# Performance work log

Hardware: AMD Instinct MI355X
Metric: run time of the kernel (lower is better)

Reference implementation:

```python
import jax, jax.numpy as jnp
import numpy as np

V, T, E, H, L = 32000, 1024, 1024, 16, 6
D = E // H
FF = 4 * E
B = 2


def _ln(x, s, b, eps=1e-5):
    m = x.mean(-1, keepdims=True)
    v = x.var(-1, keepdims=True)
    return (x - m) * jax.lax.rsqrt(v + eps) * s + b


def setup_inputs() -> dict:
    key = jax.random.key(0)
    ks = jax.random.split(key, 16)
    std = 0.02
    inp = {
        "idx": jax.random.randint(ks[0], (B, T), 0, V),
        "tok_w": jax.random.normal(ks[1], (V, E)) * std,
        "pos_emb": jax.random.normal(ks[2], (1, T, E)) * std,
        # stacked per-layer params [L, ...]
        "ln1_s": jnp.ones((L, E)), "ln1_b": jnp.zeros((L, E)),
        "wq": jax.random.normal(ks[3], (L, E, E)) * std,
        "wk": jax.random.normal(ks[4], (L, E, E)) * std,
        "wv": jax.random.normal(ks[5], (L, E, E)) * std,
        "wo": jax.random.normal(ks[6], (L, E, E)) * std,
        "bo": jnp.zeros((L, E)),
        "ln2_s": jnp.ones((L, E)), "ln2_b": jnp.zeros((L, E)),
        "w1": jax.random.normal(ks[7], (L, E, FF)) * std,
        "b1": jnp.zeros((L, FF)),
        "w2": jax.random.normal(ks[8], (L, FF, E)) * std,
        "b2": jnp.zeros((L, E)),
        "lnf_s": jnp.ones((E,)), "lnf_b": jnp.zeros((E,)),
        "head_w": jax.random.normal(ks[9], (E, V)) * std,
        "head_b": jnp.zeros((V,)),
    }
    return inp


def _gpt(idx, tok_w, pos_emb, ln1_s, ln1_b, wq, wk, wv, wo, bo,
         ln2_s, ln2_b, w1, b1, w2, b2, lnf_s, lnf_b, head_w, head_b):
    x = tok_w[idx] + pos_emb[0, :T]                      # [B,T,E]
    mask = jnp.tril(jnp.ones((T, T), dtype=bool))        # causal mask
    scale = 1.0 / np.sqrt(D)

    def step(x, p):
        l1s, l1b, q_w, k_w, v_w, o_w, o_b, l2s, l2b, f1, fb1, f2, fb2 = p
        h = _ln(x, l1s, l1b)
        q = (h @ q_w).reshape(B, T, H, D)
        k = (h @ k_w).reshape(B, T, H, D)
        v = (h @ v_w).reshape(B, T, H, D)
        att = jnp.einsum('bthd,bshd->bhts', q, k) * scale  # [B,H,T,T]
        att = jnp.where(mask, att, -jnp.inf)
        att = jax.nn.softmax(att, axis=-1)
        o = jnp.einsum('bhts,bshd->bthd', att, v).reshape(B, T, E)
        x = x + o @ o_w + o_b
        h2 = _ln(x, l2s, l2b)
        x = x + jax.nn.relu(h2 @ f1 + fb1) @ f2 + fb2
        return x, None

    params = (ln1_s, ln1_b, wq, wk, wv, wo, bo, ln2_s, ln2_b, w1, b1, w2, b2)
    x, _ = jax.lax.scan(step, x, params)
    x = _ln(x, lnf_s, lnf_b)
    return x @ head_w + head_b                           # logits [B,T,V]


def reference(idx, tok_w, pos_emb, ln1_s, ln1_b, wq, wk, wv, wo, bo,
              ln2_s, ln2_b, w1, b1, w2, b2, lnf_s, lnf_b, head_w, head_b):
    return _gpt(idx, tok_w, pos_emb, ln1_s, ln1_b, wq, wk, wv, wo, bo,
                ln2_s, ln2_b, w1, b1, w2, b2, lnf_s, lnf_b, head_w, head_b)
```

## Files before the change

### kernel.cpp

```cpp
#include <hip/hip_runtime.h>


#define T_SEQ 1024
#define E_DIM 1024
#define H_NUM 16
#define D_HEAD 64
#define L_NUM 6
#define FF_DIM 4096
#define B_NUM 2
#define M_ROWS 2048

using bf16x8 = __attribute__((ext_vector_type(8))) __bf16;
using f32x4  = __attribute__((ext_vector_type(4))) float;

__device__ __forceinline__ unsigned short f2bf(float f) {
  unsigned int u = __float_as_uint(f);
  u += 0x7fffu + ((u >> 16) & 1u);
  return (unsigned short)(u >> 16);
}

__device__ __forceinline__ void gload_lds16(const void* g, void* l) {
  __builtin_amdgcn_global_load_lds(
      (const __attribute__((address_space(1))) unsigned int*)g,
      (__attribute__((address_space(3))) unsigned int*)l, 16, 0, 0);
}

__global__ __launch_bounds__(256) void embed_k(const int* __restrict__ idx,
                                               const float* __restrict__ tok_w,
                                               const float* __restrict__ pos,
                                               float* __restrict__ x) {
  const int i = blockIdx.x;
  const int t = i & (T_SEQ - 1);
  const int tok = idx[i];
  const float4 a = ((const float4*)(tok_w + (size_t)tok * E_DIM))[threadIdx.x];
  const float4 p = ((const float4*)(pos + (size_t)t * E_DIM))[threadIdx.x];
  float4 o;
  o.x = a.x + p.x; o.y = a.y + p.y; o.z = a.z + p.z; o.w = a.w + p.w;
  ((float4*)(x + (size_t)i * E_DIM))[threadIdx.x] = o;
}

__device__ __forceinline__ void ln_body(const float* __restrict__ x,
                                        const float* __restrict__ s,
                                        const float* __restrict__ b,
                                        unsigned short* __restrict__ out,
                                        int blk) {
  const int wave = threadIdx.x >> 6, lane = threadIdx.x & 63;
  const int row = blk * 4 + wave;
  const float4* xr = (const float4*)(x + (size_t)row * E_DIM);
  float4 v[4];
  float sum = 0.f, sq = 0.f;
  #pragma unroll
  for (int i = 0; i < 4; ++i) {
    v[i] = xr[lane + 64 * i];
    sum += v[i].x + v[i].y + v[i].z + v[i].w;
    sq  += v[i].x * v[i].x + v[i].y * v[i].y + v[i].z * v[i].z + v[i].w * v[i].w;
  }
  #pragma unroll
  for (int off = 1; off < 64; off <<= 1) {
    sum += __shfl_xor(sum, off);
    sq  += __shfl_xor(sq, off);
  }
  const float mean = sum * (1.0f / E_DIM);
  const float var  = sq * (1.0f / E_DIM) - mean * mean;
  const float inv  = 1.0f / sqrtf(var + 1e-5f);
  unsigned short* orow = out + (size_t)row * E_DIM;
  #pragma unroll
  for (int i = 0; i < 4; ++i) {
    const float4 sv = ((const float4*)s)[lane + 64 * i];
    const float4 bv = ((const float4*)b)[lane + 64 * i];
    ushort4 o;
    o.x = f2bf((v[i].x - mean) * inv * sv.x + bv.x);
    o.y = f2bf((v[i].y - mean) * inv * sv.y + bv.y);
    o.z = f2bf((v[i].z - mean) * inv * sv.z + bv.z);
    o.w = f2bf((v[i].w - mean) * inv * sv.w + bv.w);
    *(ushort4*)(orow + 4 * (lane + 64 * i)) = o;
  }
}

__global__ __launch_bounds__(256) void ln_k(const float* __restrict__ x,
                                            const float* __restrict__ s,
                                            const float* __restrict__ b,
                                            unsigned short* __restrict__ out) {
  ln_body(x, s, b, out, blockIdx.x);
}

__device__ __forceinline__ void trans_body(const float* __restrict__ W,
                                           unsigned short* __restrict__ WT,
                                           int K, int N, int b,
                                           float (*tile)[33]) {
  const int nbn = N >> 5;
  const int n0 = (b % nbn) << 5, k0 = (b / nbn) << 5;
  const int tx = threadIdx.x & 31, ty = threadIdx.x >> 5;
  #pragma unroll
  for (int i = ty; i < 32; i += 8)
    tile[i][tx] = W[(size_t)(k0 + i) * N + n0 + tx];
  __syncthreads();
  #pragma unroll
  for (int i = ty; i < 32; i += 8)
    WT[(size_t)(n0 + i) * K + k0 + tx] = f2bf(tile[tx][i]);
}

__global__ __launch_bounds__(256) void ln_trans_k(
    const float* __restrict__ x, const float* __restrict__ s,
    const float* __restrict__ b, unsigned short* __restrict__ outh,
    const float* __restrict__ wq, const float* __restrict__ wk,
    const float* __restrict__ wv, const float* __restrict__ wo,
    const float* __restrict__ w1, const float* __restrict__ w2,
    unsigned short* __restrict__ wt_qkv, unsigned short* __restrict__ wt_o,
    unsigned short* __restrict__ wt_f1, unsigned short* __restrict__ wt_f2) {
  __shared__ float tile[32][33];
  const int bid = blockIdx.x;
  if (bid < 512) { ln_body(x, s, b, outh, bid); return; }
  const int tb = bid - 512;
  if (tb < 3072) {
    const int w = tb >> 10;
    const float* W = (w == 0) ? wq : (w == 1) ? wk : wv;
    trans_body(W, wt_qkv + (size_t)w * 1024 * 1024, 1024, 1024, tb & 1023, tile);
  } else if (tb < 4096) {
    trans_body(wo, wt_o, 1024, 1024, tb - 3072, tile);
  } else if (tb < 8192) {
    trans_body(w1, wt_f1, 1024, 4096, tb - 4096, tile);
  } else {
    trans_body(w2, wt_f2, 4096, 1024, tb - 8192, tile);
  }
}

__global__ __launch_bounds__(256) void lnf_trans_k(
    const float* __restrict__ x, const float* __restrict__ s,
    const float* __restrict__ b, unsigned short* __restrict__ outh,
    const float* __restrict__ head_w, unsigned short* __restrict__ wth) {
  __shared__ float tile[32][33];
  const int bid = blockIdx.x;
  if (bid < 512) { ln_body(x, s, b, outh, bid); return; }
  trans_body(head_w, wth, 1024, 32000, bid - 512, tile);
}

template<int BM, bool RELU, bool BIAS, bool RES, bool OBF16>
__global__ __launch_bounds__(256) void gemm_k(const unsigned short* __restrict__ A,
                                              const unsigned short* __restrict__ WT,
                                              const float* __restrict__ bias,
                                              const float* __restrict__ res,
                                              void* __restrict__ Cout,
                                              int ldc, int K) {
  constexpr int BN = 128;
  constexpr int BK = 64;
  constexpr int MF = BM / 32;
  constexpr int AJ = (BM * BK * 2 / 1024) / 4;
  constexpr int BJ = (BN * BK * 2 / 1024) / 4;
  constexpr int NL = AJ + BJ;
  __shared__ __align__(16) unsigned short As[2][BM][BK];
  __shared__ __align__(16) unsigned short Bs[2][BN][BK];
  const int tid = threadIdx.x;
  const int row0 = blockIdx.x * BM, col0 = blockIdx.y * BN;
  const int wave = tid >> 6, lane = tid & 63;
  const int wm = (wave >> 1) * (BM / 2), wn = (wave & 1) * 64;
  const int lr = lane & 15, lg = lane >> 4;
  const int ric = lane >> 3, sslot = lane & 7;

  auto stage = [&](int buf, int k0) {
    #pragma unroll
    for (int j = 0; j < AJ; ++j) {
      const int c = wave + 4 * j;
      const int row = c * 8 + ric;
      const int sp = sslot ^ (row & 7);
      gload_lds16(A + (size_t)(row0 + row) * K + k0 + sp * 8,
                  (char*)&As[buf][0][0] + c * 1024);
    }
    #pragma unroll
    for (int j = 0; j < BJ; ++j) {
      const int c = wave + 4 * j;
      const int row = c * 8 + ric;
      const int sp = sslot ^ (row & 7);
      gload_lds16(WT + (size_t)(col0 + row) * K + k0 + sp * 8,
                  (char*)&Bs[buf][0][0] + c * 1024);
    }
  };

  f32x4 acc[MF][4] = {};
  const int nt = K / BK;
  stage(0, 0);
  asm volatile("s_waitcnt vmcnt(0)" ::: "memory");
  __builtin_amdgcn_s_barrier();
  for (int t = 0; t < nt; ++t) {
    const int cur = t & 1;
    if (t + 1 < nt) {
      stage(cur ^ 1, (t + 1) * BK);
      asm volatile("s_waitcnt vmcnt(%0)" :: "i"(NL) : "memory");
    } else {
      asm volatile("s_waitcnt vmcnt(0)" ::: "memory");
    }
    __builtin_amdgcn_s_barrier();
    #pragma unroll
    for (int ks = 0; ks < 2; ++ks) {
      bf16x8 af[MF], bfr[4];
      #pragma unroll
      for (int m = 0; m < MF; ++m) {
        const int r = wm + m * 16 + lr;
        const int s = (ks * 4 + lg) ^ (r & 7);
        af[m] = *(const bf16x8*)((const char*)&As[cur][0][0] + r * 128 + s * 16);
      }
      #pragma unroll
      for (int n = 0; n < 4; ++n) {
        const int r = wn + n * 16 + lr;
        const int s = (ks * 4 + lg) ^ (r & 7);
        bfr[n] = *(const bf16x8*)((const char*)&Bs[cur][0][0] + r * 128 + s * 16);
      }
      #pragma unroll
      for (int m = 0; m < MF; ++m)
        #pragma unroll
        for (int n = 0; n < 4; ++n)
          acc[m][n] = __builtin_amdgcn_mfma_f32_16x16x32_bf16(af[m], bfr[n], acc[m][n], 0, 0, 0);
    }
    __builtin_amdgcn_s_barrier();
  }
  float* Cf = (float*)Cout;
  unsigned short* Cb = (unsigned short*)Cout;
  #pragma unroll
  for (int m = 0; m < MF; ++m) {
    #pragma unroll
    for (int n = 0; n < 4; ++n) {
      const int col = col0 + wn + (n << 4) + lr;
      const float bv = BIAS ? bias[col] : 0.0f;
      #pragma unroll
      for (int r = 0; r < 4; ++r) {
        const int row = row0 + wm + (m << 4) + (lg << 2) + r;
        float val = acc[m][n][r] + bv;
        if (RELU) val = fmaxf(val, 0.0f);
        if (RES)  val += res[(size_t)row * ldc + col];
        if (OBF16) Cb[(size_t)row * ldc + col] = f2bf(val);
        else       Cf[(size_t)row * ldc + col] = val;
      }
    }
  }
}

#define LOAD_AF(HALF)                                                         \
  _Pragma("unroll")                                                           \
  for (int mf = 0; mf < 4; ++mf) {                                            \
    const int rr = wm * 64 + mf * 16 + lr;                                    \
    _Pragma("unroll")                                                         \
    for (int ks = 0; ks < 2; ++ks)                                            \
      af[mf][ks] = *(const bf16x8*)&As[buf][HALF][rr]                         \
          [(((ks << 2) + lgp) ^ (rr & 7)) << 3];                              \
  }
#define LOAD_BF(HALF, DST)                                                    \
  _Pragma("unroll")                                                           \
  for (int nf = 0; nf < 2; ++nf) {                                            \
    const int rr = wn * 32 + nf * 16 + lr;                                    \
    _Pragma("unroll")                                                         \
    for (int ks = 0; ks < 2; ++ks)                                            \
      DST[nf][ks] = *(const bf16x8*)&Bs[buf][HALF][rr]                        \
          [(((ks << 2) + lgp) ^ (rr & 7)) << 3];                              \
  }
#define MFMA_Q(MH, NH, BQ)                                                    \
  __builtin_amdgcn_s_setprio(1);                                              \
  _Pragma("unroll")                                                           \
  for (int mf = 0; mf < 4; ++mf)                                              \
    _Pragma("unroll")                                                         \
    for (int nf = 0; nf < 2; ++nf) {                                          \
      acc[MH][NH][mf][nf] = __builtin_amdgcn_mfma_f32_16x16x32_bf16(          \
          af[mf][0], BQ[nf][0], acc[MH][NH][mf][nf], 0, 0, 0);                \
      acc[MH][NH][mf][nf] = __builtin_amdgcn_mfma_f32_16x16x32_bf16(          \
          af[mf][1], BQ[nf][1], acc[MH][NH][mf][nf], 0, 0, 0);                \
    }                                                                         \
  __builtin_amdgcn_s_setprio(0);

__global__ __launch_bounds__(512) void gemm8_k(
    const unsigned short* __restrict__ A, const unsigned short* __restrict__ WT,
    const float* __restrict__ bias, float* __restrict__ C,
    int ldc, int K, int mgrid) {
  constexpr int BK = 64;
  __shared__ __align__(16) unsigned short As[2][2][128][64];
  __shared__ __align__(16) unsigned short Bs[2][2][128][64];
  const int tid = threadIdx.x;
  const int wave = tid >> 6, lane = tid & 63;
  const int wm = wave >> 2, wn = wave & 3;
  const int lr = lane & 15, lgp = lane >> 4;
  const int nwg = gridDim.x;
  const int q = nwg >> 3, r = nwg & 7;
  const int xcd = blockIdx.x & 7;
  const int lgid = (xcd < r ? xcd * (q + 1) : r * (q + 1) + (xcd - r) * q)
                   + (blockIdx.x >> 3);
  const int row0 = (lgid % mgrid) * 256, col0 = (lgid / mgrid) * 256;
  const int srow = lane >> 3, sslot = lane & 7;

  auto stA = [&](int buf, int half, int k0) {
    #pragma unroll
    for (int j = 0; j < 2; ++j) {
      const int row = j * 64 + wave * 8 + srow;
      const int sp = sslot ^ (row & 7);
      gload_lds16(A + (size_t)(row0 + half * 128 + row) * K + k0 + sp * 8,
                  (char*)&As[buf][half][0][0] + j * 8192 + wave * 1024);
    }
  };
  auto stB = [&](int buf, int half, int k0) {
    #pragma unroll
    for (int j = 0; j < 2; ++j) {
      const int row = j * 64 + wave * 8 + srow;
      const int sp = sslot ^ (row & 7);
      gload_lds16(WT + (size_t)(col0 + half * 128 + row) * K + k0 + sp * 8,
                  (char*)&Bs[buf][half][0][0] + j * 8192 + wave * 1024);
    }
  };

  f32x4 acc[2][2][4][2] = {};
  bf16x8 af[4][2], bfq0[2][2], bfq1[2][2];
  const int nt = K / BK;

  stA(0, 0, 0); stB(0, 1, 0); stB(0, 0, 0); stA(0, 1, 0);
  if (nt > 1) {
    stA(1, 0, BK); stB(1, 1, BK);
    asm volatile("s_waitcnt vmcnt(4)" ::: "memory");
  } else {
    asm volatile("s_waitcnt vmcnt(0)" ::: "memory");
  }
  __builtin_amdgcn_s_barrier();

  for (int t = 0; t < nt; ++t) {
    const int buf = t & 1, nbuf = buf ^ 1;
    const int k0 = t * BK;
    LOAD_AF(0)
    LOAD_BF(0, bfq0)
    if (t + 1 < nt) { stB(nbuf, 0, k0 + BK); stA(nbuf, 1, k0 + BK); }
    MFMA_Q(0, 0, bfq0)
    LOAD_BF(1, bfq1)
    MFMA_Q(0, 1, bfq1)
    __builtin_amdgcn_s_barrier();
    LOAD_AF(1)
    if (t + 2 < nt) stA(buf, 0, k0 + 2 * BK);
    MFMA_Q(1, 1, bfq1)
    if (t + 2 < nt) stB(buf, 1, k0 + 2 * BK);
    MFMA_Q(1, 0, bfq0)
    if (t + 1 < nt) {
      if (t + 2 < nt) asm volatile("s_waitcnt vmcnt(4)" ::: "memory");
      else            asm volatile("s_waitcnt vmcnt(0)" ::: "memory");
    }
    __builtin_amdgcn_s_barrier();
  }

  #pragma unroll
  for (int mh = 0; mh < 2; ++mh)
    #pragma unroll
    for (int nh = 0; nh < 2; ++nh)
      #pragma unroll
      for (int mf = 0; mf < 4; ++mf)
        #pragma unroll
        for (int nf = 0; nf < 2; ++nf) {
          const int col = col0 + nh * 128 + wn * 32 + nf * 16 + lr;
          const float bv = bias[col];
          #pragma unroll
          for (int rr = 0; rr < 4; ++rr) {
            const int row = row0 + mh * 128 + wm * 64 + mf * 16 + lgp * 4 + rr;
            C[(size_t)row * ldc + col] = acc[mh][nh][mf][nf][rr] + bv;
          }
        }
}

#define QBLK 128
#define KBLK 64
__global__ __launch_bounds__(512) void fattn_k(const unsigned short* __restrict__ qkv,
                                               unsigned short* __restrict__ ob) {
  const int qt = (T_SEQ / QBLK - 1) - blockIdx.x;
  const int h = blockIdx.y, b = blockIdx.z;
  const int tid = threadIdx.x;
  const int wave = tid >> 6, lane = tid & 63;
  const int lr = lane & 15, lg = lane >> 4;
  const int q0 = qt * QBLK;

  __shared__ __align__(16) unsigned short Qs[QBLK][72];
  __shared__ __align__(16) unsigned short Ks[2][KBLK][64];
  __shared__ __align__(16) unsigned short Vt[2][D_HEAD][72];
  __shared__ __align__(16) unsigned short Ps[QBLK][72];

  const size_t base = (size_t)b * T_SEQ * 3072 + (size_t)h * 64;
  const int srow = tid >> 3, scol = (tid & 7) << 3;
  const int krow = wave * 8 + (lane >> 3);
  const int ksp  = (lane & 7) ^ (krow & 7);

  uint4 vreg;
  auto stage_k = [&](int buf, int s0) {
    gload_lds16(qkv + base + 1024 + (size_t)(s0 + krow) * 3072 + ksp * 8,
                (char*)&Ks[buf][0][0] + wave * 1024);
  };
  auto load_v = [&](int s0) {
    vreg = *(const uint4*)(qkv + base + 2048 + (size_t)(s0 + srow) * 3072 + scol);
  };
  auto write_v = [&](int buf) {
    const unsigned short* ws = (const unsigned short*)&vreg;
    #pragma unroll
    for (int j = 0; j < 8; ++j) Vt[buf][scol + j][srow] = ws[j];
  };

  #pragma unroll
  for (int it = 0; it < 2; ++it) {
    const int row = srow + it * 64;
    *(uint4*)&Qs[row][scol] =
        *(const uint4*)(qkv + base + (size_t)(q0 + row) * 3072 + scol);
  }
  stage_k(0, 0);
  load_v(0);
  write_v(0);
  __syncthreads();
  bf16x8 qf[2];
  #pragma unroll
  for (int ks = 0; ks < 2; ++ks)
    qf[ks] = *(const bf16x8*)&Qs[wave * 16 + lr][ks * 32 + lg * 8];

  f32x4 acc_o[4] = {};
  float mrow[4], lrow[4];
  #pragma unroll
  for (int r = 0; r < 4; ++r) { mrow[r] = -3.0e38f; lrow[r] = 0.f; }

  const int ntile = 2 * (qt + 1);
  for (int kt = 0; kt < ntile; ++kt) {
    const int s0 = kt * KBLK;
    const int cur = kt & 1;
    f32x4 sacc[4] = {};
    __builtin_amdgcn_s_setprio(1);
    #pragma unroll
    for (int ks = 0; ks < 2; ++ks) {
      #pragma unroll
      for (int nf = 0; nf < 4; ++nf) {
        const int r = nf * 16 + lr;
        bf16x8 kf = *(const bf16x8*)((const char*)&Ks[cur][0][0] +
                                     r * 128 + (((ks << 2) + lg) ^ (r & 7)) * 16);
        sacc[nf] = __builtin_amdgcn_mfma_f32_16x16x32_bf16(qf[ks], kf, sacc[nf], 0, 0, 0);
      }
    }
    __builtin_amdgcn_s_setprio(0);
    if (kt + 1 < ntile) { stage_k(cur ^ 1, s0 + KBLK); load_v(s0 + KBLK); }
    float sv[4][4];
    #pragma unroll
    for (int nf = 0; nf < 4; ++nf)
      #pragma unroll
      for (int r = 0; r < 4; ++r) sv[nf][r] = sacc[nf][r] * 0.125f;
    if (s0 + KBLK - 1 > q0) {
      #pragma unroll
      for (int nf = 0; nf < 4; ++nf) {
        const int s = s0 + nf * 16 + lr;
        #pragma unroll
        for (int r = 0; r < 4; ++r) {
          const int qq = q0 + wave * 16 + lg * 4 + r;
          if (s > qq) sv[nf][r] = -3.0e38f;
        }
      }
    }
    float p[4][4];
    #pragma unroll
    for (int r = 0; r < 4; ++r) {
      float mx = fmaxf(fmaxf(sv[0][r], sv[1][r]), fmaxf(sv[2][r], sv[3][r]));
      #pragma unroll
      for (int off = 1; off < 16; off <<= 1) mx = fmaxf(mx, __shfl_xor(mx, off));
      const float mnew = fmaxf(mrow[r], mx);
      const float alpha = __expf(mrow[r] - mnew);
      mrow[r] = mnew;
      float sum = 0.f;
      #pragma unroll
      for (int nf = 0; nf < 4; ++nf) {
        p[nf][r] = __expf(sv[nf][r] - mnew);
        sum += p[nf][r];
      }
      #pragma unroll
      for (int off = 1; off < 16; off <<= 1) sum += __shfl_xor(sum, off);
      lrow[r] = lrow[r] * alpha + sum;
      #pragma unroll
      for (int df = 0; df < 4; ++df) acc_o[df][r] *= alpha;
    }
    #pragma unroll
    for (int nf = 0; nf < 4; ++nf)
      #pragma unroll
      for (int r = 0; r < 4; ++r)
        Ps[wave * 16 + lg * 4 + r][nf * 16 + lr] = f2bf(p[nf][r]);
    __builtin_amdgcn_s_setprio(1);
    #pragma unroll
    for (int ks = 0; ks < 2; ++ks) {
      bf16x8 pa = *(const bf16x8*)&Ps[wave * 16 + lr][ks * 32 + lg * 8];
      #pragma unroll
      for (int df = 0; df < 4; ++df) {
        bf16x8 vf = *(const bf16x8*)&Vt[cur][df * 16 + lr][ks * 32 + lg * 8];
        acc_o[df] = __builtin_amdgcn_mfma_f32_16x16x32_bf16(pa, vf, acc_o[df], 0, 0, 0);
      }
    }
    __builtin_amdgcn_s_setprio(0);
    if (kt + 1 < ntile) write_v(cur ^ 1);
    __syncthreads();
  }
  #pragma unroll
  for (int r = 0; r < 4; ++r) {
    const float inv = 1.0f / lrow[r];
    const int row = q0 + wave * 16 + lg * 4 + r;
    #pragma unroll
    for (int df = 0; df < 4; ++df)
      ob[((size_t)b * T_SEQ + row) * E_DIM + h * 64 + df * 16 + lr] =
          f2bf(acc_o[df][r] * inv);
  }
}

extern "C" void kernel_launch(void* const* d_in, const int* in_sizes, int n_in,
                              void* d_out, int out_size, void* d_ws, size_t ws_size,
                              hipStream_t stream) {
  (void)in_sizes; (void)n_in; (void)out_size; (void)ws_size;
  const int*   idx    = (const int*)d_in[0];
  const float* tok_w  = (const float*)d_in[1];
  const float* pos    = (const float*)d_in[2];
  const float* ln1_s  = (const float*)d_in[3];
  const float* ln1_b  = (const float*)d_in[4];
  const float* wq     = (const float*)d_in[5];
  const float* wk     = (const float*)d_in[6];
  const float* wv     = (const float*)d_in[7];
  const float* wo     = (const float*)d_in[8];
  const float* bo     = (const float*)d_in[9];
  const float* ln2_s  = (const float*)d_in[10];
  const float* ln2_b  = (const float*)d_in[11];
  const float* w1     = (const float*)d_in[12];
  const float* b1     = (const float*)d_in[13];
  const float* w2     = (const float*)d_in[14];
  const float* b2     = (const float*)d_in[15];
  const float* lnf_s  = (const float*)d_in[16];
  const float* lnf_b  = (const float*)d_in[17];
  const float* head_w = (const float*)d_in[18];
  const float* head_b = (const float*)d_in[19];
  float* out = (float*)d_out;

  char* p = (char*)d_ws;
  float* x            = (float*)p;          p += (size_t)M_ROWS * E_DIM * 4;
  unsigned short* qkvb= (unsigned short*)p; p += (size_t)M_ROWS * 3072 * 2;
  unsigned short* h   = (unsigned short*)p; p += (size_t)M_ROWS * E_DIM * 2;
  unsigned short* obuf= (unsigned short*)p; p += (size_t)M_ROWS * E_DIM * 2;
  unsigned short* ff  = (unsigned short*)p; p += (size_t)M_ROWS * FF_DIM * 2;
  unsigned short* wt  = (unsigned short*)p; p += (size_t)3072 * E_DIM * 2;
  unsigned short* wto = (unsigned short*)p; p += (size_t)E_DIM * E_DIM * 2;
  unsigned short* wtf1= (unsigned short*)p; p += (size_t)FF_DIM * E_DIM * 2;
  unsigned short* wtf2= (unsigned short*)p; p += (size_t)E_DIM * FF_DIM * 2;
  unsigned short* wth = (unsigned short*)p; p += (size_t)32000 * E_DIM * 2;

  embed_k<<<M_ROWS, 256, 0, stream>>>(idx, tok_w, pos, x);

  for (int l = 0; l < L_NUM; ++l) {
    const size_t lEE = (size_t)l * E_DIM * E_DIM;
    const size_t lEF = (size_t)l * E_DIM * FF_DIM;
    ln_trans_k<<<12800, 256, 0, stream>>>(
        x, ln1_s + l * E_DIM, ln1_b + l * E_DIM, h,
        wq + lEE, wk + lEE, wv + lEE, wo + lEE, w1 + lEF, w2 + lEF,
        wt, wto, wtf1, wtf2);
    gemm_k<64,false,false,false,true><<<dim3(32, 24), 256, 0, stream>>>(
        h, wt, nullptr, nullptr, qkvb, 3072, E_DIM);
    fattn_k<<<dim3(T_SEQ / QBLK, H_NUM, B_NUM), 512, 0, stream>>>(qkvb, obuf);
    gemm_k<32,false,true,true,false><<<dim3(64, 8), 256, 0, stream>>>(
        obuf, wto, bo + l * E_DIM, x, x, E_DIM, E_DIM);
    ln_k<<<M_ROWS / 4, 256, 0, stream>>>(x, ln2_s + l * E_DIM, ln2_b + l * E_DIM, h);
    gemm_k<64,true,true,false,true><<<dim3(32, 32), 256, 0, stream>>>(
        h, wtf1, b1 + l * FF_DIM, nullptr, ff, FF_DIM, E_DIM);
    gemm_k<32,false,true,true,false><<<dim3(64, 8), 256, 0, stream>>>(
        ff, wtf2, b2 + l * E_DIM, x, x, E_DIM, FF_DIM);
  }

  lnf_trans_k<<<32512, 256, 0, stream>>>(x, lnf_s, lnf_b, h, head_w, wth);
  gemm8_k<<<1000, 512, 0, stream>>>(h, wth, head_b, out, 32000, E_DIM, 8);
}
```

Baseline: 1.296 ms.

## Add dedicated 512-thread FFN up-projection GEMM with 128x256 tiles and XCD-aware mapping

Replaces the generic gemm_k launch for the FF1 (bias+ReLU) projection with a new gemmup_k kernel. It uses 8 waves per block, 128x256 output tiles, double-buffered swizzled LDS loads issued directly from global memory, and prefetch interleaved with MFMA quarters. Blocks are remapped so consecutive logical tiles land on the same XCD, which should improve L2 reuse. The 256 blocks should also fill the GPU better. The cost is a hand-tuned wait-count pipeline that is fragile and more register pressure from prio/interleaving.

```diff
diff --git a/kernel.cpp b/kernel.cpp
--- a/kernel.cpp
+++ b/kernel.cpp
@@ -352,6 +352,126 @@
           for (int rr = 0; rr < 4; ++rr) {
             const int row = row0 + mh * 128 + wm * 64 + mf * 16 + lgp * 4 + rr;
             C[(size_t)row * ldc + col] = acc[mh][nh][mf][nf][rr] + bv;
+          }
+        }
+}
+
+#define LOAD_AF2(HALF)                                                        \
+  _Pragma("unroll")                                                           \
+  for (int mf = 0; mf < 2; ++mf) {                                            \
+    const int rr = wm * 32 + mf * 16 + lr;                                    \
+    _Pragma("unroll")                                                         \
+    for (int ks = 0; ks < 2; ++ks)                                            \
+      af[mf][ks] = *(const bf16x8*)&As[buf][HALF][rr]                         \
+          [(((ks << 2) + lgp) ^ (rr & 7)) << 3];                              \
+  }
+#define LOAD_BF2(HALF, DST)                                                   \
+  _Pragma("unroll")                                                           \
+  for (int nf = 0; nf < 2; ++nf) {                                            \
+    const int rr = wn * 32 + nf * 16 + lr;                                    \
+    _Pragma("unroll")                                                         \
+    for (int ks = 0; ks < 2; ++ks)                                            \
+      DST[nf][ks] = *(const bf16x8*)&Bs[buf][HALF][rr]                        \
+          [(((ks << 2) + lgp) ^ (rr & 7)) << 3];                              \
+  }
+#define MFMA_Q2(MH, NH, BQ)                                                   \
+  __builtin_amdgcn_s_setprio(1);                                              \
+  _Pragma("unroll")                                                           \
+  for (int mf = 0; mf < 2; ++mf)                                              \
+    _Pragma("unroll")                                                         \
+    for (int nf = 0; nf < 2; ++nf) {                                          \
+      acc[MH][NH][mf][nf] = __builtin_amdgcn_mfma_f32_16x16x32_bf16(          \
+          af[mf][0], BQ[nf][0], acc[MH][NH][mf][nf], 0, 0, 0);                \
+      acc[MH][NH][mf][nf] = __builtin_amdgcn_mfma_f32_16x16x32_bf16(          \
+          af[mf][1], BQ[nf][1], acc[MH][NH][mf][nf], 0, 0, 0);                \
+    }                                                                         \
+  __builtin_amdgcn_s_setprio(0);
+
+__global__ __launch_bounds__(512) void gemmup_k(
+    const unsigned short* __restrict__ A, const unsigned short* __restrict__ WT,
+    const float* __restrict__ bias, unsigned short* __restrict__ C,
+    int ldc, int K, int mgrid) {
+  constexpr int BK = 64;
+  __shared__ __align__(16) unsigned short As[2][2][64][64];
+  __shared__ __align__(16) unsigned short Bs[2][2][128][64];
+  const int tid = threadIdx.x;
+  const int wave = tid >> 6, lane = tid & 63;
+  const int wm = wave >> 2, wn = wave & 3;
+  const int lr = lane & 15, lgp = lane >> 4;
+  const int nwg = gridDim.x;
+  const int q = nwg >> 3, r = nwg & 7;
+  const int xcd = blockIdx.x & 7;
+  const int lgid = (xcd < r ? xcd * (q + 1) : r * (q + 1) + (xcd - r) * q)
+                   + (blockIdx.x >> 3);
+  const int row0 = (lgid % mgrid) * 128, col0 = (lgid / mgrid) * 256;
+  const int srow = lane >> 3, sslot = lane & 7;
+
+  auto stA2 = [&](int buf, int half, int k0) {
+    const int row = wave * 8 + srow;
+    const int sp = sslot ^ (row & 7);
+    gload_lds16(A + (size_t)(row0 + half * 64 + row) * K + k0 + sp * 8,
+                (char*)&As[buf][half][0][0] + wave * 1024);
+  };
+  auto stB2 = [&](int buf, int half, int k0) {
+    #pragma unroll
+    for (int j = 0; j < 2; ++j) {
+      const int row = j * 64 + wave * 8 + srow;
+      const int sp = sslot ^ (row & 7);
+      gload_lds16(WT + (size_t)(col0 + half * 128 + row) * K + k0 + sp * 8,
+                  (char*)&Bs[buf][half][0][0] + j * 8192 + wave * 1024);
+    }
+  };
+
+  f32x4 acc[2][2][2][2] = {};
+  bf16x8 af[2][2], bfq0[2][2], bfq1[2][2];
+  const int nt = K / BK;
+
+  stA2(0, 0, 0); stB2(0, 1, 0); stB2(0, 0, 0); stA2(0, 1, 0);
+  if (nt > 1) {
+    stA2(1, 0, BK); stB2(1, 1, BK);
+    asm volatile("s_waitcnt vmcnt(3)" ::: "memory");
+  } else {
+    asm volatile("s_waitcnt vmcnt(0)" ::: "memory");
+  }
+  __builtin_amdgcn_s_barrier();
+
+  for (int t = 0; t < nt; ++t) {
+    const int buf = t & 1, nbuf = buf ^ 1;
+    const int k0 = t * BK;
+    LOAD_AF2(0)
+    LOAD_BF2(0, bfq0)
+    if (t + 1 < nt) { stB2(nbuf, 0, k0 + BK); stA2(nbuf, 1, k0 + BK); }
+    MFMA_Q2(0, 0, bfq0)
+    LOAD_BF2(1, bfq1)
+    MFMA_Q2(0, 1, bfq1)
+    __builtin_amdgcn_s_barrier();
+    LOAD_AF2(1)
+    if (t + 2 < nt) stA2(buf, 0, k0 + 2 * BK);
+    MFMA_Q2(1, 1, bfq1)
+    if (t + 2 < nt) stB2(buf, 1, k0 + 2 * BK);
+    MFMA_Q2(1, 0, bfq0)
+    if (t + 1 < nt) {
+      if (t + 2 < nt) asm volatile("s_waitcnt vmcnt(3)" ::: "memory");
+      else            asm volatile("s_waitcnt vmcnt(0)" ::: "memory");
+    }
+    __builtin_amdgcn_s_barrier();
+  }
+
+  #pragma unroll
+  for (int mh = 0; mh < 2; ++mh)
+    #pragma unroll
+    for (int nh = 0; nh < 2; ++nh)
+      #pragma unroll
+      for (int mf = 0; mf < 2; ++mf)
+        #pragma unroll
+        for (int nf = 0; nf < 2; ++nf) {
+          const int col = col0 + nh * 128 + wn * 32 + nf * 16 + lr;
+          const float bv = bias[col];
+          #pragma unroll
+          for (int rr = 0; rr < 4; ++rr) {
+            const int row = row0 + mh * 64 + wm * 32 + mf * 16 + lgp * 4 + rr;
+            C[(size_t)row * ldc + col] =
+                f2bf(fmaxf(acc[mh][nh][mf][nf][rr] + bv, 0.0f));
           }
         }
 }
@@ -549,8 +669,8 @@
     gemm_k<32,false,true,true,false><<<dim3(64, 8), 256, 0, stream>>>(
         obuf, wto, bo + l * E_DIM, x, x, E_DIM, E_DIM);
     ln_k<<<M_ROWS / 4, 256, 0, stream>>>(x, ln2_s + l * E_DIM, ln2_b + l * E_DIM, h);
-    gemm_k<64,true,true,false,true><<<dim3(32, 32), 256, 0, stream>>>(
-        h, wtf1, b1 + l * FF_DIM, nullptr, ff, FF_DIM, E_DIM);
+    gemmup_k<<<256, 512, 0, stream>>>(
+        h, wtf1, b1 + l * FF_DIM, ff, FF_DIM, E_DIM, 16);
     gemm_k<32,false,true,true,false><<<dim3(64, 8), 256, 0, stream>>>(
         ff, wtf2, b2 + l * E_DIM, x, x, E_DIM, FF_DIM);
   }
```

New measurement: 1.269 ms. 2.1% less time.
